# Kernel tuning notes

Hardware: AMD Instinct MI355X
Metric: run time of the kernel (lower is better)

Reference implementation:

```python
import jax, jax.numpy as jnp
import numpy as np

OUT_FEATURES = 3


def setup_inputs() -> dict:
    key = jax.random.key(0)
    k1, k2 = jax.random.split(key)
    x = jax.random.normal(k1, (4096, 49152), dtype=jnp.float32)
    weight = jax.random.normal(k2, (16384, 6), dtype=jnp.float32) * 0.1
    return {"x": x, "weight": weight}


def _build_blocks(weight):
    # weight: [n, 6] -> upper-triangular M per block, softplus on the diagonal
    n = weight.shape[0]
    sp = jax.nn.softplus
    z = jnp.zeros((n,), weight.dtype)
    row0 = jnp.stack([sp(weight[:, 0]), weight[:, 1], weight[:, 2]], axis=-1)
    row1 = jnp.stack([z, sp(weight[:, 3]), weight[:, 4]], axis=-1)
    row2 = jnp.stack([z, z, sp(weight[:, 5])], axis=-1)
    M = jnp.stack([row0, row1, row2], axis=1)  # [n, 3, 3]
    # wBlock = M^T @ M per block (symmetric PSD)
    return jnp.einsum('nki,nkj->nij', M, M)  # [n, 3, 3]


def reference(x, weight):
    # x: [B, 3*n], weight: [n, 6]
    n = weight.shape[0]
    wBlock = _build_blocks(weight)  # [n, 3, 3]
    xb = x.reshape(x.shape[0], n, 3)  # [B, n, 3]
    # F.linear: x_slice @ wBlock^T, summed over blocks into out[:, 0:3]
    out3 = jnp.einsum('bni,nji->bj', xb, wBlock)  # [B, 3]
    if OUT_FEATURES == 3:
        return out3
    out = jnp.zeros((x.shape[0], OUT_FEATURES), x.dtype)
    return out.at[:, :3].set(out3)
```

## Files before the change

kernel.cpp:

```cpp
#include <hip/hip_runtime.h>
#include <math.h>

static constexpr int NB   = 16384;
static constexpr int COLS = NB * 3;
static constexpr int VEC  = COLS / 4;
static constexpr int ROWS = 4096;
static constexpr int TPB  = 256;

__device__ __forceinline__ float softplus_f(float v) {
    return log1pf(expf(-fabsf(v))) + fmaxf(v, 0.0f);
}

__global__ void build_wexp(const float* __restrict__ w,
                           float* __restrict__ W0,
                           float* __restrict__ W1,
                           float* __restrict__ W2) {
    int n = blockIdx.x * blockDim.x + threadIdx.x;
    if (n >= NB) return;
    float w0 = w[n * 6 + 0], w1 = w[n * 6 + 1], w2 = w[n * 6 + 2];
    float w3 = w[n * 6 + 3], w4 = w[n * 6 + 4], w5 = w[n * 6 + 5];
    float a = softplus_f(w0), b = w1, c = w2;
    float d = softplus_f(w3), e = w4, f = softplus_f(w5);
    float W00 = a * a;
    float W01 = a * b;
    float W02 = a * c;
    float W11 = b * b + d * d;
    float W12 = b * c + d * e;
    float W22 = c * c + e * e + f * f;
    int base = 3 * n;
    W0[base + 0] = W00; W0[base + 1] = W01; W0[base + 2] = W02;
    W1[base + 0] = W01; W1[base + 1] = W11; W1[base + 2] = W12;
    W2[base + 0] = W02; W2[base + 1] = W12; W2[base + 2] = W22;
}

__global__ __launch_bounds__(TPB) void row_reduce(
    const float4* __restrict__ x,
    const float4* __restrict__ W0,
    const float4* __restrict__ W1,
    const float4* __restrict__ W2,
    float* __restrict__ out) {
    const int row = blockIdx.x;
    const float4* __restrict__ xr = x + (size_t)row * VEC;

    float a0 = 0.f, a1 = 0.f, a2 = 0.f;
    #pragma unroll 4
    for (int v = threadIdx.x; v < VEC; v += TPB) {
        float4 xv = xr[v];
        float4 q0 = W0[v];
        float4 q1 = W1[v];
        float4 q2 = W2[v];
        a0 = fmaf(xv.x, q0.x, fmaf(xv.y, q0.y, fmaf(xv.z, q0.z, fmaf(xv.w, q0.w, a0))));
        a1 = fmaf(xv.x, q1.x, fmaf(xv.y, q1.y, fmaf(xv.z, q1.z, fmaf(xv.w, q1.w, a1))));
        a2 = fmaf(xv.x, q2.x, fmaf(xv.y, q2.y, fmaf(xv.z, q2.z, fmaf(xv.w, q2.w, a2))));
    }

    #pragma unroll
    for (int off = 32; off > 0; off >>= 1) {
        a0 += __shfl_down(a0, off);
        a1 += __shfl_down(a1, off);
        a2 += __shfl_down(a2, off);
    }

    __shared__ float red[TPB / 64][3];
    const int lane = threadIdx.x & 63;
    const int wv   = threadIdx.x >> 6;
    if (lane == 0) {
        red[wv][0] = a0;
        red[wv][1] = a1;
        red[wv][2] = a2;
    }
    __syncthreads();
    if (threadIdx.x == 0) {
        float s0 = 0.f, s1 = 0.f, s2 = 0.f;
        #pragma unroll
        for (int i = 0; i < TPB / 64; ++i) {
            s0 += red[i][0];
            s1 += red[i][1];
            s2 += red[i][2];
        }
        out[row * 3 + 0] = s0;
        out[row * 3 + 1] = s1;
        out[row * 3 + 2] = s2;
    }
}

extern "C" void kernel_launch(void* const* d_in, const int* in_sizes, int n_in,
                              void* d_out, int out_size, void* d_ws, size_t ws_size,
                              hipStream_t stream) {
    const float* x = (const float*)d_in[0];
    const float* w = (const float*)d_in[1];
    float* out = (float*)d_out;

    float* W0 = (float*)d_ws;
    float* W1 = W0 + COLS;
    float* W2 = W1 + COLS;

    build_wexp<<<(NB + TPB - 1) / TPB, TPB, 0, stream>>>(w, W0, W1, W2);
    row_reduce<<<ROWS, TPB, 0, stream>>>(
        (const float4*)x, (const float4*)W0, (const float4*)W1,
        (const float4*)W2, out);
}
```

Baseline: 1.053 ms.

## Split columns into chunks with register-resident weights and a two-pass reduction

The GEMV is restructured so each block owns one column chunk and a tile of 32 rows. The block loads its W0/W1/W2 slice into registers once and reuses it across those rows, instead of re-reading the weights for every row. Per-wave partial sums go to workspace, and a separate kernel reduces them into the output. The cost is higher register pressure from 12 float4 weight slots per thread, one extra kernel launch, and extra workspace traffic. The x stream is unchanged and likely remains the bottleneck.

```diff
diff --git a/kernel.cpp b/kernel.cpp
--- a/kernel.cpp
+++ b/kernel.cpp
@@ -6,6 +6,14 @@
 static constexpr int VEC  = COLS / 4;
 static constexpr int ROWS = 4096;
 static constexpr int TPB  = 256;
+
+static constexpr int CHUNKS    = 12;
+static constexpr int CHUNK_VEC = VEC / CHUNKS;
+static constexpr int SLOTS     = CHUNK_VEC / TPB;
+static constexpr int ROW_TILE  = 32;
+static constexpr int ROW_TILES = ROWS / ROW_TILE;
+static constexpr int WAVES     = TPB / 64;
+static constexpr int NPART     = CHUNKS * WAVES;
 
 __device__ __forceinline__ float softplus_f(float v) {
     return log1pf(expf(-fabsf(v))) + fmaxf(v, 0.0f);
@@ -33,55 +41,83 @@
     W2[base + 0] = W02; W2[base + 1] = W12; W2[base + 2] = W22;
 }
 
-__global__ __launch_bounds__(TPB) void row_reduce(
+__global__ __launch_bounds__(TPB) void partial_gemv(
     const float4* __restrict__ x,
     const float4* __restrict__ W0,
     const float4* __restrict__ W1,
     const float4* __restrict__ W2,
-    float* __restrict__ out) {
-    const int row = blockIdx.x;
-    const float4* __restrict__ xr = x + (size_t)row * VEC;
+    float* __restrict__ partial) {
+    const int chunk = blockIdx.x % CHUNKS;
+    const int rt    = blockIdx.x / CHUNKS;
+    const int t     = threadIdx.x;
+    const int vbase = chunk * CHUNK_VEC;
 
-    float a0 = 0.f, a1 = 0.f, a2 = 0.f;
-    #pragma unroll 4
-    for (int v = threadIdx.x; v < VEC; v += TPB) {
-        float4 xv = xr[v];
-        float4 q0 = W0[v];
-        float4 q1 = W1[v];
-        float4 q2 = W2[v];
-        a0 = fmaf(xv.x, q0.x, fmaf(xv.y, q0.y, fmaf(xv.z, q0.z, fmaf(xv.w, q0.w, a0))));
-        a1 = fmaf(xv.x, q1.x, fmaf(xv.y, q1.y, fmaf(xv.z, q1.z, fmaf(xv.w, q1.w, a1))));
-        a2 = fmaf(xv.x, q2.x, fmaf(xv.y, q2.y, fmaf(xv.z, q2.z, fmaf(xv.w, q2.w, a2))));
+    float4 q0[SLOTS], q1[SLOTS], q2[SLOTS];
+    #pragma unroll
+    for (int s = 0; s < SLOTS; ++s) {
+        const int v = vbase + t + s * TPB;
+        q0[s] = W0[v];
+        q1[s] = W1[v];
+        q2[s] = W2[v];
     }
 
+    const int r0   = rt * ROW_TILE;
+    const int lane = t & 63;
+    const int wv   = t >> 6;
+
+    for (int r = 0; r < ROW_TILE; ++r) {
+        const float4* __restrict__ xr =
+            x + (size_t)(r0 + r) * VEC + vbase;
+
+        float4 xv[SLOTS];
+        #pragma unroll
+        for (int s = 0; s < SLOTS; ++s) xv[s] = xr[t + s * TPB];
+
+        float a0 = 0.f, a1 = 0.f, a2 = 0.f;
+        #pragma unroll
+        for (int s = 0; s < SLOTS; ++s) {
+            a0 = fmaf(xv[s].x, q0[s].x,
+                 fmaf(xv[s].y, q0[s].y,
+                 fmaf(xv[s].z, q0[s].z,
+                 fmaf(xv[s].w, q0[s].w, a0))));
+            a1 = fmaf(xv[s].x, q1[s].x,
+                 fmaf(xv[s].y, q1[s].y,
+                 fmaf(xv[s].z, q1[s].z,
+                 fmaf(xv[s].w, q1[s].w, a1))));
+            a2 = fmaf(xv[s].x, q2[s].x,
+                 fmaf(xv[s].y, q2[s].y,
+                 fmaf(xv[s].z, q2[s].z,
+                 fmaf(xv[s].w, q2[s].w, a2))));
+        }
+
+        #pragma unroll
+        for (int off = 32; off > 0; off >>= 1) {
+            a0 += __shfl_down(a0, off);
+            a1 += __shfl_down(a1, off);
+            a2 += __shfl_down(a2, off);
+        }
+
+        if (lane == 0) {
+            float* p = partial +
+                ((size_t)(r0 + r) * NPART + chunk * WAVES + wv) * 3;
+            p[0] = a0;
+            p[1] = a1;
+            p[2] = a2;
+        }
+    }
+}
+
+__global__ __launch_bounds__(TPB) void reduce_partials(
+    const float* __restrict__ partial, float* __restrict__ out) {
+    const int tid = blockIdx.x * blockDim.x + threadIdx.x;
+    if (tid >= ROWS * 3) return;
+    const int row = tid / 3;
+    const int j   = tid % 3;
+    const float* p = partial + (size_t)row * NPART * 3 + j;
+    float s = 0.f;
     #pragma unroll
-    for (int off = 32; off > 0; off >>= 1) {
-        a0 += __shfl_down(a0, off);
-        a1 += __shfl_down(a1, off);
-        a2 += __shfl_down(a2, off);
-    }
-
-    __shared__ float red[TPB / 64][3];
-    const int lane = threadIdx.x & 63;
-    const int wv   = threadIdx.x >> 6;
-    if (lane == 0) {
-        red[wv][0] = a0;
-        red[wv][1] = a1;
-        red[wv][2] = a2;
-    }
-    __syncthreads();
-    if (threadIdx.x == 0) {
-        float s0 = 0.f, s1 = 0.f, s2 = 0.f;
-        #pragma unroll
-        for (int i = 0; i < TPB / 64; ++i) {
-            s0 += red[i][0];
-            s1 += red[i][1];
-            s2 += red[i][2];
-        }
-        out[row * 3 + 0] = s0;
-        out[row * 3 + 1] = s1;
-        out[row * 3 + 2] = s2;
-    }
+    for (int i = 0; i < NPART; ++i) s += p[i * 3];
+    out[tid] = s;
 }
 
 extern "C" void kernel_launch(void* const* d_in, const int* in_sizes, int n_in,
@@ -94,9 +130,11 @@
     float* W0 = (float*)d_ws;
     float* W1 = W0 + COLS;
     float* W2 = W1 + COLS;
+    float* partial = W2 + COLS;
 
     build_wexp<<<(NB + TPB - 1) / TPB, TPB, 0, stream>>>(w, W0, W1, W2);
-    row_reduce<<<ROWS, TPB, 0, stream>>>(
+    partial_gemv<<<CHUNKS * ROW_TILES, TPB, 0, stream>>>(
         (const float4*)x, (const float4*)W0, (const float4*)W1,
-        (const float4*)W2, out);
+        (const float4*)W2, partial);
+    reduce_partials<<<(ROWS * 3 + TPB - 1) / TPB, TPB, 0, stream>>>(partial, out);
 }
```

After: 1.009 ms. -4.2%, faster.
